# Optimization experiments

Measured on AMD Instinct MI355X. Metric: run time of the kernel, lower is better.

The kernel has to match this reference:

```python
import jax, jax.numpy as jnp
import numpy as np

B, T, C, H = 4, 2048, 1024, 16
D = C // H  # head dim = 64


def setup_inputs() -> dict:
    key = jax.random.key(0)
    ks = jax.random.split(key, 5)
    s = 0.02
    return {
        "x": jax.random.normal(ks[0], (B, T, C), dtype=jnp.float32),
        "W_attn": jax.random.normal(ks[1], (C, 3 * C), dtype=jnp.float32) * s,
        "b_attn": jnp.zeros((3 * C,), dtype=jnp.float32),
        "W_proj": jax.random.normal(ks[2], (C, C), dtype=jnp.float32) * s,
        "b_proj": jnp.zeros((C,), dtype=jnp.float32),
    }


def reference(x, W_attn, b_attn, W_proj, b_proj):
    # qkv projection: [B,T,3C]
    qkv = x @ W_attn + b_attn
    q, k, v = jnp.split(qkv, 3, axis=-1)
    # [B,T,C] -> [B,H,T,D]
    def heads(t):
        return t.reshape(B, T, H, D).transpose(0, 2, 1, 3)
    q, k, v = heads(q), heads(k), heads(v)
    # scaled scores with causal mask, materialized [B,H,T,T] as in original
    att = jnp.einsum('bhqd,bhkd->bhqk', q, k) * (1.0 / np.sqrt(D))
    causal = jnp.tril(jnp.ones((T, T), dtype=bool))
    att = jnp.where(causal[None, None], att, -jnp.inf)
    att = jax.nn.softmax(att, axis=-1)
    y = jnp.einsum('bhqk,bhkd->bhqd', att, v)  # [B,H,T,D]
    y = y.transpose(0, 2, 1, 3).reshape(B, T, C)
    y = y @ W_proj + b_proj
    # original also returns present=(k,v); it is a pure pass-through cache
    return y
```

## Files before the change

### kernel.cpp

```cpp
#include <hip/hip_runtime.h>


typedef unsigned short u16;
typedef unsigned int u32;
typedef __attribute__((ext_vector_type(8))) unsigned short u16x8;
typedef __attribute__((ext_vector_type(4))) unsigned short u16x4;
typedef __attribute__((ext_vector_type(8))) short short8;
typedef __attribute__((ext_vector_type(4))) float f32x4;

__device__ inline u16 f2bf(float f) {
  unsigned u = __float_as_uint(f);
  u = (u + 0x7FFF + ((u >> 16) & 1)) >> 16;
  return (u16)u;
}

__device__ inline f32x4 mfma16(short8 a, short8 b, f32x4 c) {
  return __builtin_amdgcn_mfma_f32_16x16x32_bf16(a, b, c, 0, 0, 0);
}

__device__ inline void tw_tile(const float* __restrict__ in,
                               u16* __restrict__ outT, int R, int Cc,
                               int c0, int r0, int tid, u16 (*t)[65]) {
  int a = tid & 63, w = tid >> 6;
#pragma unroll
  for (int j = 0; j < 16; ++j) {
    int r = w + j * 4;
    t[r][a] = f2bf(in[(size_t)(r0 + r) * Cc + c0 + a]);
  }
  __syncthreads();
#pragma unroll
  for (int j = 0; j < 16; ++j) {
    int c = w + j * 4;
    outT[(size_t)(c0 + c) * R + r0 + a] = t[a][c];
  }
}

__global__ __launch_bounds__(256) void k_prep(const float* __restrict__ x,
                                              u16* __restrict__ xb,
                                              const float* __restrict__ Wa,
                                              u16* __restrict__ wta,
                                              const float* __restrict__ Wp,
                                              u16* __restrict__ wtp) {
  __shared__ u16 t[64][65];
  const int id = blockIdx.x, tid = threadIdx.x;
  if (id < 8192) {
    int i = (id * 256 + tid) * 4;
    float4 v = *(const float4*)(x + i);
    u16x4 o = {f2bf(v.x), f2bf(v.y), f2bf(v.z), f2bf(v.w)};
    *(u16x4*)(xb + i) = o;
  } else if (id < 8960) {
    int q = id - 8192;
    tw_tile(Wa, wta, 1024, 3072, (q % 48) * 64, (q / 48) * 64, tid, t);
  } else {
    int q = id - 8960;
    tw_tile(Wp, wtp, 1024, 1024, (q % 16) * 64, (q / 16) * 64, tid, t);
  }
}

template <int OUTBF, int QSCALE, int VT>
__global__ __launch_bounds__(256) void gemm_bt(const u16* __restrict__ A,
                                               const u16* __restrict__ Bt,
                                               const float* __restrict__ bias,
                                               u16* __restrict__ outb,
                                               float* __restrict__ outf,
                                               u16* __restrict__ vtout,
                                               int M, int N, int K) {
  __shared__ u16 As[128 * 64];
  __shared__ u16 Bs[128 * 64];
  const int nx = gridDim.x, ny = gridDim.y;
  int id0 = blockIdx.x + blockIdx.y * nx;
  int nwg = nx * ny;
  int q8 = nwg >> 3, x8 = id0 & 7, c8 = id0 >> 3;
  int id = x8 * q8 + c8;
  int gs = 8 * ny, grp = id / gs, rem = id % gs;
  const int m0 = (grp * 8 + (rem & 7)) * 128, n0 = (rem >> 3) * 128;

  const int tid = threadIdx.x, wave = tid >> 6, lane = tid & 63;
  const int quad = lane >> 4, l16 = lane & 15;
  const int wm = (wave & 1) * 64, wn = (wave >> 1) * 64;
  const int lrow = lane >> 3;
  const int lch = lane & 7;
  const int slot = lch ^ lrow;
  const u16* sA[4];
  const u16* sB[4];
  int offA[4], offB[4];
#pragma unroll
  for (int j = 0; j < 4; ++j) {
    int r = wave * 32 + j * 8;
    sA[j] = A + (size_t)(m0 + r + lrow) * K + lch * 8;
    sB[j] = Bt + (size_t)(n0 + r + lrow) * K + lch * 8;
    offA[j] = (r + lrow) * 64 + slot * 8;
    offB[j] = offA[j];
  }
  u16x8 ra[4], rb[4];
#pragma unroll
  for (int j = 0; j < 4; ++j) {
    ra[j] = *(const u16x8*)(sA[j]);
    rb[j] = *(const u16x8*)(sB[j]);
  }
  f32x4 acc[4][4] = {};
  for (int kt = 0; kt < K; kt += 64) {
    __syncthreads();
#pragma unroll
    for (int j = 0; j < 4; ++j) {
      *(u16x8*)&As[offA[j]] = ra[j];
      *(u16x8*)&Bs[offB[j]] = rb[j];
    }
    __syncthreads();
    if (kt + 64 < K) {
#pragma unroll
      for (int j = 0; j < 4; ++j) {
        ra[j] = *(const u16x8*)(sA[j] + kt + 64);
        rb[j] = *(const u16x8*)(sB[j] + kt + 64);
      }
    }
    const int sl = l16 & 7;
#pragma unroll
    for (int ks = 0; ks < 2; ++ks) {
      short8 af[4], bf[4];
#pragma unroll
      for (int mt = 0; mt < 4; ++mt)
        af[mt] = *(const short8*)(As + (wm + mt * 16 + l16) * 64 +
                                  ((ks * 4 + quad) ^ sl) * 8);
#pragma unroll
      for (int nt = 0; nt < 4; ++nt)
        bf[nt] = *(const short8*)(Bs + (wn + nt * 16 + l16) * 64 +
                                  ((ks * 4 + quad) ^ sl) * 8);
#pragma unroll
      for (int mt = 0; mt < 4; ++mt)
#pragma unroll
        for (int nt = 0; nt < 4; ++nt)
          acc[mt][nt] = mfma16(af[mt], bf[nt], acc[mt][nt]);
    }
  }
#pragma unroll
  for (int nt = 0; nt < 4; ++nt) {
    int col = n0 + wn + nt * 16 + l16;
    float bv = bias[col];
    if (VT && col >= 2048) {
      const int hd = col - 2048;
#pragma unroll
      for (int mt = 0; mt < 4; ++mt) {
        int rowb = m0 + wm + mt * 16 + quad * 4;
        int bb = rowb >> 11, t0 = rowb & 2047;
        u16x4 pk;
#pragma unroll
        for (int r = 0; r < 4; ++r) pk[r] = f2bf(acc[mt][nt][r] + bv);
        *(u16x4*)(vtout + ((size_t)(bb << 10) + hd) * 2048 + t0) = pk;
      }
    } else {
#pragma unroll
      for (int mt = 0; mt < 4; ++mt) {
        int rowb = m0 + wm + mt * 16 + quad * 4;
#pragma unroll
        for (int r = 0; r < 4; ++r) {
          float v = acc[mt][nt][r] + bv;
          if (QSCALE && col < 1024) v *= 0.18033688f;
          if (OUTBF)
            outb[(size_t)(rowb + r) * N + col] = f2bf(v);
          else
            outf[(size_t)(rowb + r) * N + col] = v;
        }
      }
    }
  }
}

#define ATP 72
__global__ __launch_bounds__(256) void attn(const u16* __restrict__ qkv,
                                            const u16* __restrict__ vt,
                                            u16* __restrict__ y) {
  __shared__ u16 shm[256 * ATP];
  u16* Qs = shm;
  u16* Ks = shm + 128 * ATP;
  u16* Vs = shm + 192 * ATP;
  const int p = blockIdx.x, h = blockIdx.y, b = blockIdx.z;
  const int tid = threadIdx.x, wave = tid >> 6, lane = tid & 63;
  const int quad = lane >> 4, l16 = lane & 15;
  const u16* Qg = qkv + (size_t)b * 2048 * 3072 + h * 64;
  const u16* Kg = Qg + 1024;
  const u16* Vtg = vt + (size_t)(b * 16 + h) * 64 * 2048;
  const int srow0 = tid >> 3, scol0 = (tid & 7) * 8;
  u16* Pw0 = Qs + (wave * 16) * ATP;
  u16* Pw1 = Qs + (64 + wave * 16) * ATP;
  short8 ones_f;
#pragma unroll
  for (int j = 0; j < 8; ++j) ones_f[j] = 0x3F80;

  for (int half = 0; half < 2; ++half) {
    const int qb = half ? (15 - p) : p;
    const int q0 = qb * 128;
    const int nkt = 2 * qb + 2;
    const u16* kp0 = Kg + (size_t)srow0 * 3072 + scol0;
    const u16* kp1 = kp0 + 32 * 3072;
    const u16* vp0 = Vtg + (size_t)srow0 * 2048 + scol0;
    const u16* vp1 = vp0 + 32 * 2048;
    u16x8 qr0 = *(const u16x8*)(Qg + (size_t)(q0 + srow0) * 3072 + scol0);
    u16x8 qr1 = *(const u16x8*)(Qg + (size_t)(q0 + srow0 + 32) * 3072 + scol0);
    u16x8 qr2 = *(const u16x8*)(Qg + (size_t)(q0 + srow0 + 64) * 3072 + scol0);
    u16x8 qr3 = *(const u16x8*)(Qg + (size_t)(q0 + srow0 + 96) * 3072 + scol0);
    u16x8 kreg0 = *(const u16x8*)kp0, kreg1 = *(const u16x8*)kp1;
    u16x8 vreg0 = *(const u16x8*)vp0, vreg1 = *(const u16x8*)vp1;
    __syncthreads();
    *(u16x8*)&Qs[(size_t)srow0 * ATP + scol0] = qr0;
    *(u16x8*)&Qs[(size_t)(srow0 + 32) * ATP + scol0] = qr1;
    *(u16x8*)&Qs[(size_t)(srow0 + 64) * ATP + scol0] = qr2;
    *(u16x8*)&Qs[(size_t)(srow0 + 96) * ATP + scol0] = qr3;
    *(u16x8*)&Ks[(size_t)srow0 * ATP + scol0] = kreg0;
    *(u16x8*)&Ks[(size_t)(srow0 + 32) * ATP + scol0] = kreg1;
    *(u16x8*)&Vs[(size_t)srow0 * ATP + scol0] = vreg0;
    *(u16x8*)&Vs[(size_t)(srow0 + 32) * ATP + scol0] = vreg1;
    __syncthreads();
    short8 qf0a = *(const short8*)&Qs[(wave * 16 + l16) * ATP + quad * 8];
    short8 qf1a = *(const short8*)&Qs[(wave * 16 + l16) * ATP + 32 + quad * 8];
    short8 qf0b = *(const short8*)&Qs[(64 + wave * 16 + l16) * ATP + quad * 8];
    short8 qf1b = *(const short8*)&Qs[(64 + wave * 16 + l16) * ATP + 32 + quad * 8];

    f32x4 lacc0 = {}, lacc1 = {};
    f32x4 o0[4] = {}, o1[4] = {};

    auto tile = [&](int kt, int g0mode, bool g1mask) {
      if (kt > 0) {
        __syncthreads();
        *(u16x8*)&Ks[(size_t)srow0 * ATP + scol0] = kreg0;
        *(u16x8*)&Ks[(size_t)(srow0 + 32) * ATP + scol0] = kreg1;
        *(u16x8*)&Vs[(size_t)srow0 * ATP + scol0] = vreg0;
        *(u16x8*)&Vs[(size_t)(srow0 + 32) * ATP + scol0] = vreg1;
        __syncthreads();
      }
      if (kt + 1 < nkt) {
        kreg0 = *(const u16x8*)(kp0 += 64 * 3072);
        kreg1 = *(const u16x8*)(kp1 += 64 * 3072);
        vreg0 = *(const u16x8*)(vp0 += 64);
        vreg1 = *(const u16x8*)(vp1 += 64);
      }

      f32x4 s0[4] = {}, s1[4] = {};
#pragma unroll
      for (int mt = 0; mt < 4; ++mt) {
        short8 kf0 = *(const short8*)&Ks[(mt * 16 + l16) * ATP + quad * 8];
        short8 kf1 = *(const short8*)&Ks[(mt * 16 + l16) * ATP + 32 + quad * 8];
        if (g0mode < 2) {
          s0[mt] = mfma16(kf0, qf0a, s0[mt]);
          s0[mt] = mfma16(kf1, qf1a, s0[mt]);
        }
        s1[mt] = mfma16(kf0, qf0b, s1[mt]);
        s1[mt] = mfma16(kf1, qf1b, s1[mt]);
      }

      if (g0mode < 2) {
        const int qrow = q0 + wave * 16 + l16;
#pragma unroll
        for (int mt = 0; mt < 4; ++mt) {
          float pe[4];
#pragma unroll
          for (int r = 0; r < 4; ++r) {
            float pv = __builtin_amdgcn_exp2f(s0[mt][r]);
            if (g0mode == 1) {
              int kcol = kt * 64 + mt * 16 + quad * 4 + r;
              if (kcol > qrow) pv = 0.f;
            }
            pe[r] = pv;
          }
          u32 lo = __builtin_amdgcn_perm(__float_as_uint(pe[1]),
                                         __float_as_uint(pe[0]), 0x07060302u);
          u32 hi = __builtin_amdgcn_perm(__float_as_uint(pe[3]),
                                         __float_as_uint(pe[2]), 0x07060302u);
          uint2 pk = {lo, hi};
          *(uint2*)&Pw0[l16 * ATP + mt * 16 + quad * 4] = pk;
        }
      }
      {
        const int qrow = q0 + 64 + wave * 16 + l16;
#pragma unroll
        for (int mt = 0; mt < 4; ++mt) {
          float pe[4];
#pragma unroll
          for (int r = 0; r < 4; ++r) {
            float pv = __builtin_amdgcn_exp2f(s1[mt][r]);
            if (g1mask) {
              int kcol = kt * 64 + mt * 16 + quad * 4 + r;
              if (kcol > qrow) pv = 0.f;
            }
            pe[r] = pv;
          }
          u32 lo = __builtin_amdgcn_perm(__float_as_uint(pe[1]),
                                         __float_as_uint(pe[0]), 0x07060302u);
          u32 hi = __builtin_amdgcn_perm(__float_as_uint(pe[3]),
                                         __float_as_uint(pe[2]), 0x07060302u);
          uint2 pk = {lo, hi};
          *(uint2*)&Pw1[l16 * ATP + mt * 16 + quad * 4] = pk;
        }
      }

#pragma unroll
      for (int ks = 0; ks < 2; ++ks) {
        short8 pf0, pf1;
        if (g0mode < 2) {
          pf0 = *(const short8*)&Pw0[l16 * ATP + ks * 32 + quad * 8];
          lacc0 = mfma16(pf0, ones_f, lacc0);
        }
        pf1 = *(const short8*)&Pw1[l16 * ATP + ks * 32 + quad * 8];
        lacc1 = mfma16(pf1, ones_f, lacc1);
#pragma unroll
        for (int dt = 0; dt < 4; ++dt) {
          short8 vf = *(const short8*)&Vs[(dt * 16 + l16) * ATP + ks * 32 + quad * 8];
          if (g0mode < 2) o0[dt] = mfma16(pf0, vf, o0[dt]);
          o1[dt] = mfma16(pf1, vf, o1[dt]);
        }
      }
    };

    for (int kt = 0; kt < nkt - 2; ++kt) tile(kt, 0, false);
    tile(nkt - 2, 1, false);
    tile(nkt - 1, 2, true);

    size_t rb0 = (size_t)b * 2048 + q0 + wave * 16 + quad * 4;
#pragma unroll
    for (int r = 0; r < 4; ++r) {
      float inv = 1.f / lacc0[r];
#pragma unroll
      for (int dt = 0; dt < 4; ++dt)
        y[(rb0 + r) * 1024 + h * 64 + dt * 16 + l16] = f2bf(o0[dt][r] * inv);
    }
    size_t rb1 = rb0 + 64;
#pragma unroll
    for (int r = 0; r < 4; ++r) {
      float inv = 1.f / lacc1[r];
#pragma unroll
      for (int dt = 0; dt < 4; ++dt)
        y[(rb1 + r) * 1024 + h * 64 + dt * 16 + l16] = f2bf(o1[dt][r] * inv);
    }
  }
}

extern "C" void kernel_launch(void* const* d_in, const int* in_sizes, int n_in,
                              void* d_out, int out_size, void* d_ws, size_t ws_size,
                              hipStream_t stream) {
  const float* x = (const float*)d_in[0];
  const float* W_attn = (const float*)d_in[1];
  const float* b_attn = (const float*)d_in[2];
  const float* W_proj = (const float*)d_in[3];
  const float* b_proj = (const float*)d_in[4];
  float* out = (float*)d_out;
  char* ws = (char*)d_ws;
  u16* xb  = (u16*)(ws);
  u16* wta = (u16*)(ws + 16777216);
  u16* wtp = (u16*)(ws + 23068672);
  u16* qkv = (u16*)(ws + 25165824);
  u16* vt  = (u16*)(ws + 75497472);
  u16* y   = (u16*)(ws + 92274688);

  k_prep<<<dim3(9216), 256, 0, stream>>>(x, xb, W_attn, wta, W_proj, wtp);
  gemm_bt<1, 1, 1><<<dim3(64, 24), 256, 0, stream>>>(xb, wta, b_attn, qkv, nullptr, vt, 8192, 3072, 1024);
  attn<<<dim3(8, 16, 4), 256, 0, stream>>>(qkv, vt, y);
  gemm_bt<0, 0, 0><<<dim3(64, 8), 256, 0, stream>>>(y, wtp, b_proj, nullptr, out, nullptr, 8192, 1024, 1024);
}
```

Before: 238.8 us.

## Fuse x fp32-to-bf16 conversion into QKV GEMM and double-buffer attention K/V

The separate elementwise pass that converted x to bf16 in the prep kernel is removed. The QKV GEMM now loads fp32 x directly and converts it in registers while prefetching. This saves one write and one read of a 16 MB bf16 buffer, but the GEMM reads A as fp32, so the 24 column blocks fetch twice the A bytes. The attention kernel also double-buffers K/V tiles in shared memory, which drops one barrier per tile and prefetches two tiles ahead, at the cost of more LDS.

```diff
diff --git a/kernel.cpp b/kernel.cpp
--- a/kernel.cpp
+++ b/kernel.cpp
@@ -14,6 +14,13 @@
   return (u16)u;
 }
 
+__device__ inline u16x8 cvt8(float4 a, float4 b) {
+  u16x8 o;
+  o[0] = f2bf(a.x); o[1] = f2bf(a.y); o[2] = f2bf(a.z); o[3] = f2bf(a.w);
+  o[4] = f2bf(b.x); o[5] = f2bf(b.y); o[6] = f2bf(b.z); o[7] = f2bf(b.w);
+  return o;
+}
+
 __device__ inline f32x4 mfma16(short8 a, short8 b, f32x4 c) {
   return __builtin_amdgcn_mfma_f32_16x16x32_bf16(a, b, c, 0, 0, 0);
 }
@@ -35,30 +42,23 @@
   }
 }
 
-__global__ __launch_bounds__(256) void k_prep(const float* __restrict__ x,
-                                              u16* __restrict__ xb,
-                                              const float* __restrict__ Wa,
+__global__ __launch_bounds__(256) void k_prep(const float* __restrict__ Wa,
                                               u16* __restrict__ wta,
                                               const float* __restrict__ Wp,
                                               u16* __restrict__ wtp) {
   __shared__ u16 t[64][65];
   const int id = blockIdx.x, tid = threadIdx.x;
-  if (id < 8192) {
-    int i = (id * 256 + tid) * 4;
-    float4 v = *(const float4*)(x + i);
-    u16x4 o = {f2bf(v.x), f2bf(v.y), f2bf(v.z), f2bf(v.w)};
-    *(u16x4*)(xb + i) = o;
-  } else if (id < 8960) {
-    int q = id - 8192;
-    tw_tile(Wa, wta, 1024, 3072, (q % 48) * 64, (q / 48) * 64, tid, t);
+  if (id < 768) {
+    tw_tile(Wa, wta, 1024, 3072, (id % 48) * 64, (id / 48) * 64, tid, t);
   } else {
-    int q = id - 8960;
+    int q = id - 768;
     tw_tile(Wp, wtp, 1024, 1024, (q % 16) * 64, (q / 16) * 64, tid, t);
   }
 }
 
-template <int OUTBF, int QSCALE, int VT>
+template <int OUTBF, int QSCALE, int VT, int AF32>
 __global__ __launch_bounds__(256) void gemm_bt(const u16* __restrict__ A,
+                                               const float* __restrict__ Af,
                                                const u16* __restrict__ Bt,
                                                const float* __restrict__ bias,
                                                u16* __restrict__ outb,
@@ -82,12 +82,16 @@
   const int lch = lane & 7;
   const int slot = lch ^ lrow;
   const u16* sA[4];
+  const float* sAf[4];
   const u16* sB[4];
   int offA[4], offB[4];
 #pragma unroll
   for (int j = 0; j < 4; ++j) {
     int r = wave * 32 + j * 8;
-    sA[j] = A + (size_t)(m0 + r + lrow) * K + lch * 8;
+    if (AF32)
+      sAf[j] = Af + (size_t)(m0 + r + lrow) * K + lch * 8;
+    else
+      sA[j] = A + (size_t)(m0 + r + lrow) * K + lch * 8;
     sB[j] = Bt + (size_t)(n0 + r + lrow) * K + lch * 8;
     offA[j] = (r + lrow) * 64 + slot * 8;
     offB[j] = offA[j];
@@ -95,7 +99,13 @@
   u16x8 ra[4], rb[4];
 #pragma unroll
   for (int j = 0; j < 4; ++j) {
-    ra[j] = *(const u16x8*)(sA[j]);
+    if (AF32) {
+      float4 a0 = *(const float4*)(sAf[j]);
+      float4 a1 = *(const float4*)(sAf[j] + 4);
+      ra[j] = cvt8(a0, a1);
+    } else {
+      ra[j] = *(const u16x8*)(sA[j]);
+    }
     rb[j] = *(const u16x8*)(sB[j]);
   }
   f32x4 acc[4][4] = {};
@@ -110,7 +120,13 @@
     if (kt + 64 < K) {
 #pragma unroll
       for (int j = 0; j < 4; ++j) {
-        ra[j] = *(const u16x8*)(sA[j] + kt + 64);
+        if (AF32) {
+          float4 a0 = *(const float4*)(sAf[j] + kt + 64);
+          float4 a1 = *(const float4*)(sAf[j] + kt + 68);
+          ra[j] = cvt8(a0, a1);
+        } else {
+          ra[j] = *(const u16x8*)(sA[j] + kt + 64);
+        }
         rb[j] = *(const u16x8*)(sB[j] + kt + 64);
       }
     }
@@ -170,10 +186,8 @@
 __global__ __launch_bounds__(256) void attn(const u16* __restrict__ qkv,
                                             const u16* __restrict__ vt,
                                             u16* __restrict__ y) {
-  __shared__ u16 shm[256 * ATP];
+  __shared__ u16 shm[384 * ATP];
   u16* Qs = shm;
-  u16* Ks = shm + 128 * ATP;
-  u16* Vs = shm + 192 * ATP;
   const int p = blockIdx.x, h = blockIdx.y, b = blockIdx.z;
   const int tid = threadIdx.x, wave = tid >> 6, lane = tid & 63;
   const int quad = lane >> 4, l16 = lane & 15;
@@ -191,25 +205,35 @@
     const int qb = half ? (15 - p) : p;
     const int q0 = qb * 128;
     const int nkt = 2 * qb + 2;
-    const u16* kp0 = Kg + (size_t)srow0 * 3072 + scol0;
-    const u16* kp1 = kp0 + 32 * 3072;
-    const u16* vp0 = Vtg + (size_t)srow0 * 2048 + scol0;
-    const u16* vp1 = vp0 + 32 * 2048;
+    auto kadr0 = [&](int t) { return Kg + (size_t)(64 * t + srow0) * 3072 + scol0; };
+    auto vadr0 = [&](int t) { return Vtg + (size_t)srow0 * 2048 + 64 * t + scol0; };
     u16x8 qr0 = *(const u16x8*)(Qg + (size_t)(q0 + srow0) * 3072 + scol0);
     u16x8 qr1 = *(const u16x8*)(Qg + (size_t)(q0 + srow0 + 32) * 3072 + scol0);
     u16x8 qr2 = *(const u16x8*)(Qg + (size_t)(q0 + srow0 + 64) * 3072 + scol0);
     u16x8 qr3 = *(const u16x8*)(Qg + (size_t)(q0 + srow0 + 96) * 3072 + scol0);
-    u16x8 kreg0 = *(const u16x8*)kp0, kreg1 = *(const u16x8*)kp1;
-    u16x8 vreg0 = *(const u16x8*)vp0, vreg1 = *(const u16x8*)vp1;
+    u16x8 kreg0 = *(const u16x8*)(kadr0(0));
+    u16x8 kreg1 = *(const u16x8*)(kadr0(0) + 32 * 3072);
+    u16x8 vreg0 = *(const u16x8*)(vadr0(0));
+    u16x8 vreg1 = *(const u16x8*)(vadr0(0) + 32 * 2048);
     __syncthreads();
     *(u16x8*)&Qs[(size_t)srow0 * ATP + scol0] = qr0;
     *(u16x8*)&Qs[(size_t)(srow0 + 32) * ATP + scol0] = qr1;
     *(u16x8*)&Qs[(size_t)(srow0 + 64) * ATP + scol0] = qr2;
     *(u16x8*)&Qs[(size_t)(srow0 + 96) * ATP + scol0] = qr3;
-    *(u16x8*)&Ks[(size_t)srow0 * ATP + scol0] = kreg0;
-    *(u16x8*)&Ks[(size_t)(srow0 + 32) * ATP + scol0] = kreg1;
-    *(u16x8*)&Vs[(size_t)srow0 * ATP + scol0] = vreg0;
-    *(u16x8*)&Vs[(size_t)(srow0 + 32) * ATP + scol0] = vreg1;
+    {
+      u16* Kb = shm + 128 * ATP;
+      u16* Vb = Kb + 64 * ATP;
+      *(u16x8*)&Kb[(size_t)srow0 * ATP + scol0] = kreg0;
+      *(u16x8*)&Kb[(size_t)(srow0 + 32) * ATP + scol0] = kreg1;
+      *(u16x8*)&Vb[(size_t)srow0 * ATP + scol0] = vreg0;
+      *(u16x8*)&Vb[(size_t)(srow0 + 32) * ATP + scol0] = vreg1;
+    }
+    if (nkt > 1) {
+      kreg0 = *(const u16x8*)(kadr0(1));
+      kreg1 = *(const u16x8*)(kadr0(1) + 32 * 3072);
+      vreg0 = *(const u16x8*)(vadr0(1));
+      vreg1 = *(const u16x8*)(vadr0(1) + 32 * 2048);
+    }
     __syncthreads();
     short8 qf0a = *(const short8*)&Qs[(wave * 16 + l16) * ATP + quad * 8];
     short8 qf1a = *(const short8*)&Qs[(wave * 16 + l16) * ATP + 32 + quad * 8];
@@ -220,20 +244,23 @@
     f32x4 o0[4] = {}, o1[4] = {};
 
     auto tile = [&](int kt, int g0mode, bool g1mask) {
-      if (kt > 0) {
-        __syncthreads();
-        *(u16x8*)&Ks[(size_t)srow0 * ATP + scol0] = kreg0;
-        *(u16x8*)&Ks[(size_t)(srow0 + 32) * ATP + scol0] = kreg1;
-        *(u16x8*)&Vs[(size_t)srow0 * ATP + scol0] = vreg0;
-        *(u16x8*)&Vs[(size_t)(srow0 + 32) * ATP + scol0] = vreg1;
-        __syncthreads();
-      }
+      if (kt > 0) __syncthreads();
       if (kt + 1 < nkt) {
-        kreg0 = *(const u16x8*)(kp0 += 64 * 3072);
-        kreg1 = *(const u16x8*)(kp1 += 64 * 3072);
-        vreg0 = *(const u16x8*)(vp0 += 64);
-        vreg1 = *(const u16x8*)(vp1 += 64);
-      }
+        u16* Kw = shm + (128 + 128 * ((kt + 1) & 1)) * ATP;
+        u16* Vw = Kw + 64 * ATP;
+        *(u16x8*)&Kw[(size_t)srow0 * ATP + scol0] = kreg0;
+        *(u16x8*)&Kw[(size_t)(srow0 + 32) * ATP + scol0] = kreg1;
+        *(u16x8*)&Vw[(size_t)srow0 * ATP + scol0] = vreg0;
+        *(u16x8*)&Vw[(size_t)(srow0 + 32) * ATP + scol0] = vreg1;
+      }
+      if (kt + 2 < nkt) {
+        kreg0 = *(const u16x8*)(kadr0(kt + 2));
+        kreg1 = *(const u16x8*)(kadr0(kt + 2) + 32 * 3072);
+        vreg0 = *(const u16x8*)(vadr0(kt + 2));
+        vreg1 = *(const u16x8*)(vadr0(kt + 2) + 32 * 2048);
+      }
+      const u16* Ks = shm + (128 + 128 * (kt & 1)) * ATP;
+      const u16* Vs = Ks + 64 * ATP;
 
       f32x4 s0[4] = {}, s1[4] = {};
 #pragma unroll
@@ -344,15 +371,14 @@
   const float* b_proj = (const float*)d_in[4];
   float* out = (float*)d_out;
   char* ws = (char*)d_ws;
-  u16* xb  = (u16*)(ws);
   u16* wta = (u16*)(ws + 16777216);
   u16* wtp = (u16*)(ws + 23068672);
   u16* qkv = (u16*)(ws + 25165824);
   u16* vt  = (u16*)(ws + 75497472);
   u16* y   = (u16*)(ws + 92274688);
 
-  k_prep<<<dim3(9216), 256, 0, stream>>>(x, xb, W_attn, wta, W_proj, wtp);
-  gemm_bt<1, 1, 1><<<dim3(64, 24), 256, 0, stream>>>(xb, wta, b_attn, qkv, nullptr, vt, 8192, 3072, 1024);
+  k_prep<<<dim3(1024), 256, 0, stream>>>(W_attn, wta, W_proj, wtp);
+  gemm_bt<1, 1, 1, 1><<<dim3(64, 24), 256, 0, stream>>>(nullptr, x, wta, b_attn, qkv, nullptr, vt, 8192, 3072, 1024);
   attn<<<dim3(8, 16, 4), 256, 0, stream>>>(qkv, vt, y);
-  gemm_bt<0, 0, 0><<<dim3(64, 8), 256, 0, stream>>>(y, wtp, b_proj, nullptr, out, nullptr, 8192, 1024, 1024);
-}
+  gemm_bt<0, 0, 0, 0><<<dim3(64, 8), 256, 0, stream>>>(y, nullptr, wtp, b_proj, nullptr, out, nullptr, 8192, 1024, 1024);
+}
```

After: 251.8 us. +5.4%, slower.
